# Kernel optimization log

Hardware: AMD Instinct MI355X
Metric: run time of the kernel (lower is better)

## Reference

```python
import jax, jax.numpy as jnp
import numpy as np

B, Q, K, D, H = 8, 128, 1024, 256, 256


def setup_inputs() -> dict:
    key = jax.random.key(0)
    ks = jax.random.split(key, 7)
    queries = jax.random.normal(ks[0], (B, Q, D), dtype=jnp.float32)
    keys = jax.random.normal(ks[1], (B, K, D), dtype=jnp.float32)
    values = jax.random.normal(ks[2], (B, K, D), dtype=jnp.float32)
    W_q = jax.random.normal(ks[3], (H, D), dtype=jnp.float32) * (1.0 / np.sqrt(D))
    W_k = jax.random.normal(ks[4], (H, D), dtype=jnp.float32) * (1.0 / np.sqrt(D))
    w_v = jax.random.normal(ks[5], (H,), dtype=jnp.float32) * (1.0 / np.sqrt(H))
    valid_lens = jax.random.randint(ks[6], (B,), 0, K, dtype=jnp.int64)
    return {"queries": queries, "keys": keys, "values": values,
            "W_q": W_q, "W_k": W_k, "w_v": w_v, "valid_lens": valid_lens}


def reference(queries, keys, values, W_q, W_k, w_v, valid_lens):
    # Linear projections (bias=False): [B,Q,H], [B,K,H]
    q = jnp.einsum("bqd,hd->bqh", queries, W_q)
    k = jnp.einsum("bkd,hd->bkh", keys, W_k)
    # Broadcast add -> tanh -> reduce with w_v: scores [B,Q,K]
    features = jnp.tanh(q[:, :, None, :] + k[:, None, :, :])  # [B,Q,K,H]
    scores = jnp.einsum("bqkh,h->bqk", features, w_v)
    # Masked softmax over K: positions >= valid_len get -1e9
    mask = jnp.arange(K)[None, None, :] < valid_lens[:, None, None]
    scores = jnp.where(mask, scores, jnp.float32(-1e9))
    attn = jax.nn.softmax(scores, axis=-1)  # [B,Q,K]
    # Dropout p=0.0 (eval): identity. bmm(attn, values) -> [B,Q,Dv]
    return jnp.einsum("bqk,bkv->bqv", attn, values)
```

## Files before the change

kernel.cpp:

```cpp
#include <hip/hip_runtime.h>

#define BB 8
#define QQ 128
#define KK 1024
#define DD 256
#define HH 256

#define KSP 32
#define KCH 32

#define ZSP 4
#define RTOT (BB * QQ + BB * KK)
#define PSTRIDE ((size_t)RTOT * HH)

#define TWO_LOG2E     2.8853900817779268f
#define NEG_TWO_LOG2E -2.8853900817779268f

__global__ __launch_bounds__(256) void proj_kernel(const float* __restrict__ queries,
                                                   const float* __restrict__ keys,
                                                   const float* __restrict__ Wq,
                                                   const float* __restrict__ Wk,
                                                   const int* __restrict__ vlen,
                                                   float* __restrict__ pp) {
    const int r0 = blockIdx.x * 64;
    const bool isQ = (r0 < BB * QQ);
    if (!isQ) {
        const int kb = (r0 - BB * QQ) >> 6;
        const int b  = kb >> 4;
        const int k0 = (kb & 15) << 6;
        if (k0 >= vlen[b]) return;
    }

    __shared__ float smem[192 * 68];
    float (*As)[68] = (float(*)[68])smem;
    float (*Ws)[68] = (float(*)[68])(smem + 64 * 68);

    const int t  = threadIdx.x;
    const int tr = t & 15;
    const int th = t >> 4;
    const int h0 = blockIdx.y * 128;
    const int dc = blockIdx.z * 64;
    const float* A = isQ ? (queries + (size_t)r0 * DD)
                         : (keys + (size_t)(r0 - BB * QQ) * DD);
    const float* W = isQ ? Wq : Wk;

#pragma unroll
    for (int i = 0; i < 4; ++i) {
        int fi  = t + 256 * i;
        int row = fi >> 4;
        int c4  = (fi & 15) << 2;
        *(float4*)&As[row][c4] = *(const float4*)&A[(size_t)row * DD + dc + c4];
    }
#pragma unroll
    for (int i = 0; i < 8; ++i) {
        int fi  = t + 256 * i;
        int row = fi >> 4;
        int c4  = (fi & 15) << 2;
        *(float4*)&Ws[row][c4] = *(const float4*)&W[(size_t)(h0 + row) * DD + dc + c4];
    }
    __syncthreads();

    float acc[4][8] = {};
#pragma unroll 2
    for (int dd = 0; dd < 64; dd += 4) {
        float4 a4[4], w4[8];
#pragma unroll
        for (int i = 0; i < 4; ++i) a4[i] = *(float4*)&As[tr + 16 * i][dd];
#pragma unroll
        for (int j = 0; j < 8; ++j) w4[j] = *(float4*)&Ws[th + 16 * j][dd];
#pragma unroll
        for (int i = 0; i < 4; ++i)
#pragma unroll
            for (int j = 0; j < 8; ++j) {
                acc[i][j] += a4[i].x * w4[j].x + a4[i].y * w4[j].y +
                             a4[i].z * w4[j].z + a4[i].w * w4[j].w;
            }
    }
    __syncthreads();

    float (*Ob)[132] = (float(*)[132])smem;
#pragma unroll
    for (int i = 0; i < 4; ++i)
#pragma unroll
        for (int j = 0; j < 8; ++j)
            Ob[tr + 16 * i][th + 16 * j] = TWO_LOG2E * acc[i][j];
    __syncthreads();

    float* outp = pp + (size_t)blockIdx.z * PSTRIDE + (size_t)r0 * HH + h0;
#pragma unroll
    for (int i = 0; i < 8; ++i) {
        int fi  = t + 256 * i;
        int row = fi >> 5;
        int c4  = (fi & 31) << 2;
        *(float4*)&outp[(size_t)row * HH + c4] = *(float4*)&Ob[row][c4];
    }
}

__global__ __launch_bounds__(256) void combine_kernel(const float* __restrict__ pp,
                                                      const int* __restrict__ vlen,
                                                      float* __restrict__ ppc) {
    const int row = blockIdx.x * 4 + (threadIdx.x >> 6);
    const int l   = threadIdx.x & 63;
    if (row >= BB * QQ) {
        const int rk = row - BB * QQ;
        const int b  = rk >> 10;
        const int k  = rk & (KK - 1);
        if (k >= vlen[b]) return;
    }
    const float* base = pp + (size_t)row * HH + (l << 2);
    float4 v0 = *(const float4*)base;
    float4 v1 = *(const float4*)(base + PSTRIDE);
    float4 v2 = *(const float4*)(base + 2 * PSTRIDE);
    float4 v3 = *(const float4*)(base + 3 * PSTRIDE);
    float4 s;
    s.x = __builtin_amdgcn_exp2f((v0.x + v1.x) + (v2.x + v3.x));
    s.y = __builtin_amdgcn_exp2f((v0.y + v1.y) + (v2.y + v3.y));
    s.z = __builtin_amdgcn_exp2f((v0.z + v1.z) + (v2.z + v3.z));
    s.w = __builtin_amdgcn_exp2f((v0.w + v1.w) + (v2.w + v3.w));
    *(float4*)&ppc[(size_t)row * HH + (l << 2)] = s;
}

__global__ __launch_bounds__(512, 4) void scoreav_kernel(const float* __restrict__ ppc,
                                                         const float* __restrict__ wv,
                                                         const int* __restrict__ vlen,
                                                         const float* __restrict__ V,
                                                         float* __restrict__ partial,
                                                         float* __restrict__ psum) {
    int id = blockIdx.x;
    int b = 0;
    bool found = false;
#pragma unroll
    for (int bb = 0; bb < BB; ++bb) {
        if (!found) {
            int v = vlen[bb];
            int cnt = ((v == 0) ? KSP : ((v + KCH - 1) / KCH)) * 4;
            if (id < cnt) { b = bb; found = true; }
            else id -= cnt;
        }
    }
    if (!found) return;
    const int ksb = id >> 2;
    const int q0  = (id & 3) * 32;
    const int k0  = ksb * KCH;
    const int vl  = vlen[b];

    __shared__ float st[2][32][260];
    __shared__ float pT[KCH][36];
    float* red = &st[0][0][0];

    const int t = threadIdx.x;
    const int w = t >> 6;
    const int l = t & 63;
    const int ql = l & 7;
    const int kl = l >> 3;

    float acc[4][4] = {};

    if (vl > 0) {
#pragma unroll
        for (int i = 0; i < 8; ++i) {
            int fi  = t + 512 * i;
            int row = fi >> 6;
            int c4  = (fi & 63) << 2;
            size_t gr = (row < 32) ? (size_t)(b * QQ + q0 + row)
                                   : (size_t)(BB * QQ + b * KK + k0 + row - 32);
            *(float4*)&st[row >> 5][row & 31][c4] =
                *(const float4*)&ppc[gr * HH + c4];
        }
        __syncthreads();

        const int hw = 32 * w;
#pragma unroll
        for (int hh = 0; hh < 32; hh += 4) {
            const float4 w4 = *(const float4*)&wv[hw + hh];
            const float* wa = (const float*)&w4;
            float4 q4[4], k4[4];
#pragma unroll
            for (int i = 0; i < 4; ++i) q4[i] = *(float4*)&st[0][ql + 8 * i][hw + hh];
#pragma unroll
            for (int j = 0; j < 4; ++j) k4[j] = *(float4*)&st[1][kl + 8 * j][hw + hh];
#pragma unroll
            for (int i = 0; i < 4; ++i) {
                const float* qa = (const float*)&q4[i];
#pragma unroll
                for (int j = 0; j < 4; ++j) {
                    const float* ka = (const float*)&k4[j];
#pragma unroll
                    for (int c = 0; c < 4; ++c) {
                        float d = __builtin_fmaf(qa[c], ka[c], 1.0f);
                        acc[i][j] += wa[c] * __builtin_amdgcn_rcpf(d);
                    }
                }
            }
        }
        __syncthreads();

#pragma unroll
        for (int i = 0; i < 4; ++i)
#pragma unroll
            for (int j = 0; j < 4; ++j)
                red[w * 1056 + (ql + 8 * i) * 33 + (kl + 8 * j)] = acc[i][j];
    }
    __syncthreads();

    float pvv[2];
#pragma unroll
    for (int u = 0; u < 2; ++u) {
        int n = t + 512 * u;
        int q = n >> 5, k = n & 31;
        float s = 0.f;
        if (vl > 0) {
#pragma unroll
            for (int ww = 0; ww < 8; ++ww) s += red[ww * 1056 + q * 33 + k];
        }
        int kg = k0 + k;
        float pv;
        if (vl == 0) pv = 1.0f;
        else pv = (kg < vl) ? __builtin_amdgcn_exp2f(NEG_TWO_LOG2E * s) : 0.0f;
        pT[k][q] = pv;
        pvv[u] = pv;
    }
    float s0 = pvv[0], s1 = pvv[1];
#pragma unroll
    for (int off = 1; off < 32; off <<= 1) {
        s0 += __shfl_xor(s0, off);
        s1 += __shfl_xor(s1, off);
    }
    if ((l & 31) == 0) {
        int qa = 2 * w + (l >> 5);
        psum[((size_t)ksb * BB + b) * QQ + q0 + qa]      = s0;
        psum[((size_t)ksb * BB + b) * QQ + q0 + qa + 16] = s1;
    }
    __syncthreads();

    const float* VB = V + ((size_t)b * KK + k0) * DD;
    const int d4 = (t & 63) << 2;
    const int qg = w << 2;
    float4 a4[4] = {};
#pragma unroll 4
    for (int k = 0; k < KCH; ++k) {
        float4 v4 = *(const float4*)&VB[(size_t)k * DD + d4];
        float4 p4 = *(float4*)&pT[k][qg];
        a4[0].x += p4.x * v4.x; a4[0].y += p4.x * v4.y; a4[0].z += p4.x * v4.z; a4[0].w += p4.x * v4.w;
        a4[1].x += p4.y * v4.x; a4[1].y += p4.y * v4.y; a4[1].z += p4.y * v4.z; a4[1].w += p4.y * v4.w;
        a4[2].x += p4.z * v4.x; a4[2].y += p4.z * v4.y; a4[2].z += p4.z * v4.z; a4[2].w += p4.z * v4.w;
        a4[3].x += p4.w * v4.x; a4[3].y += p4.w * v4.y; a4[3].z += p4.w * v4.z; a4[3].w += p4.w * v4.w;
    }
#pragma unroll
    for (int qi = 0; qi < 4; ++qi) {
        int q = q0 + qg + qi;
        *(float4*)&partial[(((size_t)ksb * BB + b) * QQ + q) * DD + d4] = a4[qi];
    }
}

__global__ __launch_bounds__(256) void av_reduce(const float* __restrict__ partial,
                                                 const float* __restrict__ psum,
                                                 const int* __restrict__ vlen,
                                                 float* __restrict__ out) {
    const int i  = blockIdx.x * 256 + threadIdx.x;
    const int bq = i >> 6;
    const int b  = bq >> 7;
    const int vl = vlen[b];
    const int nch = (vl == 0) ? KSP : ((vl + KCH - 1) / KCH);

    const float4* p4 = (const float4*)partial;
    const int stride4 = BB * QQ * DD / 4;

    float S = 0.f;
    float4 s = {0.f, 0.f, 0.f, 0.f};
    int ks = 0;
    for (; ks + 4 <= nch; ks += 4) {
        float Sa = psum[(size_t)(ks + 0) * (BB * QQ) + bq];
        float Sb = psum[(size_t)(ks + 1) * (BB * QQ) + bq];
        float Sc = psum[(size_t)(ks + 2) * (BB * QQ) + bq];
        float Sd = psum[(size_t)(ks + 3) * (BB * QQ) + bq];
        float4 x0 = p4[(size_t)(ks + 0) * stride4 + i];
        float4 x1 = p4[(size_t)(ks + 1) * stride4 + i];
        float4 x2 = p4[(size_t)(ks + 2) * stride4 + i];
        float4 x3 = p4[(size_t)(ks + 3) * stride4 + i];
        S += (Sa + Sb) + (Sc + Sd);
        s.x += (x0.x + x1.x) + (x2.x + x3.x);
        s.y += (x0.y + x1.y) + (x2.y + x3.y);
        s.z += (x0.z + x1.z) + (x2.z + x3.z);
        s.w += (x0.w + x1.w) + (x2.w + x3.w);
    }
    for (; ks < nch; ++ks) {
        S += psum[(size_t)ks * (BB * QQ) + bq];
        float4 x = p4[(size_t)ks * stride4 + i];
        s.x += x.x; s.y += x.y; s.z += x.z; s.w += x.w;
    }

    const float inv = 1.0f / S;
    s.x *= inv; s.y *= inv; s.z *= inv; s.w *= inv;
    ((float4*)out)[i] = s;
}

extern "C" void kernel_launch(void* const* d_in, const int* in_sizes, int n_in,
                              void* d_out, int out_size, void* d_ws, size_t ws_size,
                              hipStream_t stream) {
    const float* queries = (const float*)d_in[0];
    const float* keys    = (const float*)d_in[1];
    const float* values  = (const float*)d_in[2];
    const float* W_q     = (const float*)d_in[3];
    const float* W_k     = (const float*)d_in[4];
    const float* w_v     = (const float*)d_in[5];
    const int*   vlen    = (const int*)d_in[6];
    float* out = (float*)d_out;

    float* ws      = (float*)d_ws;
    float* pp      = ws;
    float* ppc     = pp + (size_t)ZSP * PSTRIDE;
    float* psum    = ppc + PSTRIDE;
    float* partial = psum + (size_t)KSP * BB * QQ;

    proj_kernel<<<dim3(RTOT / 64, HH / 128, ZSP), 256, 0, stream>>>(
        queries, keys, W_q, W_k, vlen, pp);

    combine_kernel<<<dim3(RTOT / 4, 1, 1), 256, 0, stream>>>(pp, vlen, ppc);

    scoreav_kernel<<<dim3(KSP * 4 * BB, 1, 1), 512, 0, stream>>>(
        ppc, w_v, vlen, values, partial, psum);

    av_reduce<<<dim3(BB * QQ * DD / 4 / 256, 1, 1), 256, 0, stream>>>(
        partial, psum, vlen, out);
}
```

Measured before the change: 129.8 us.

## Process two key chunks per score block and shrink projection tile

The score/AV kernel now loops over two 32-key chunks per block, accumulating the AV partials and softmax sums in registers, which halves the number of key splits and the partial/psum traffic the reduce kernel must read. The projection kernel's H tile drops from 128 to 64, doubling its grid and cutting per-thread accumulators to raise parallelism and occupancy. The cost is fewer, longer score blocks with extra barriers, and the projection's shared loads of the A tile are no longer shared across as many outputs.

```diff
diff --git a/kernel.cpp b/kernel.cpp
--- a/kernel.cpp
+++ b/kernel.cpp
@@ -6,7 +6,7 @@
 #define DD 256
 #define HH 256
 
-#define KSP 32
+#define NSC 16
 #define KCH 32
 
 #define ZSP 4
@@ -31,14 +31,14 @@
         if (k0 >= vlen[b]) return;
     }
 
-    __shared__ float smem[192 * 68];
+    __shared__ float smem[2 * 64 * 68];
     float (*As)[68] = (float(*)[68])smem;
     float (*Ws)[68] = (float(*)[68])(smem + 64 * 68);
 
     const int t  = threadIdx.x;
     const int tr = t & 15;
     const int th = t >> 4;
-    const int h0 = blockIdx.y * 128;
+    const int h0 = blockIdx.y * 64;
     const int dc = blockIdx.z * 64;
     const float* A = isQ ? (queries + (size_t)r0 * DD)
                          : (keys + (size_t)(r0 - BB * QQ) * DD);
@@ -50,48 +50,42 @@
         int row = fi >> 4;
         int c4  = (fi & 15) << 2;
         *(float4*)&As[row][c4] = *(const float4*)&A[(size_t)row * DD + dc + c4];
-    }
-#pragma unroll
-    for (int i = 0; i < 8; ++i) {
+        *(float4*)&Ws[row][c4] = *(const float4*)&W[(size_t)(h0 + row) * DD + dc + c4];
+    }
+    __syncthreads();
+
+    float acc[4][4] = {};
+#pragma unroll 2
+    for (int dd = 0; dd < 64; dd += 4) {
+        float4 a4[4], w4[4];
+#pragma unroll
+        for (int i = 0; i < 4; ++i) a4[i] = *(float4*)&As[tr + 16 * i][dd];
+#pragma unroll
+        for (int j = 0; j < 4; ++j) w4[j] = *(float4*)&Ws[th + 16 * j][dd];
+#pragma unroll
+        for (int i = 0; i < 4; ++i)
+#pragma unroll
+            for (int j = 0; j < 4; ++j) {
+                acc[i][j] += a4[i].x * w4[j].x + a4[i].y * w4[j].y +
+                             a4[i].z * w4[j].z + a4[i].w * w4[j].w;
+            }
+    }
+    __syncthreads();
+
+    float (*Ob)[68] = (float(*)[68])smem;
+#pragma unroll
+    for (int i = 0; i < 4; ++i)
+#pragma unroll
+        for (int j = 0; j < 4; ++j)
+            Ob[tr + 16 * i][th + 16 * j] = TWO_LOG2E * acc[i][j];
+    __syncthreads();
+
+    float* outp = pp + (size_t)blockIdx.z * PSTRIDE + (size_t)r0 * HH + h0;
+#pragma unroll
+    for (int i = 0; i < 4; ++i) {
         int fi  = t + 256 * i;
         int row = fi >> 4;
         int c4  = (fi & 15) << 2;
-        *(float4*)&Ws[row][c4] = *(const float4*)&W[(size_t)(h0 + row) * DD + dc + c4];
-    }
-    __syncthreads();
-
-    float acc[4][8] = {};
-#pragma unroll 2
-    for (int dd = 0; dd < 64; dd += 4) {
-        float4 a4[4], w4[8];
-#pragma unroll
-        for (int i = 0; i < 4; ++i) a4[i] = *(float4*)&As[tr + 16 * i][dd];
-#pragma unroll
-        for (int j = 0; j < 8; ++j) w4[j] = *(float4*)&Ws[th + 16 * j][dd];
-#pragma unroll
-        for (int i = 0; i < 4; ++i)
-#pragma unroll
-            for (int j = 0; j < 8; ++j) {
-                acc[i][j] += a4[i].x * w4[j].x + a4[i].y * w4[j].y +
-                             a4[i].z * w4[j].z + a4[i].w * w4[j].w;
-            }
-    }
-    __syncthreads();
-
-    float (*Ob)[132] = (float(*)[132])smem;
-#pragma unroll
-    for (int i = 0; i < 4; ++i)
-#pragma unroll
-        for (int j = 0; j < 8; ++j)
-            Ob[tr + 16 * i][th + 16 * j] = TWO_LOG2E * acc[i][j];
-    __syncthreads();
-
-    float* outp = pp + (size_t)blockIdx.z * PSTRIDE + (size_t)r0 * HH + h0;
-#pragma unroll
-    for (int i = 0; i < 8; ++i) {
-        int fi  = t + 256 * i;
-        int row = fi >> 5;
-        int c4  = (fi & 31) << 2;
         *(float4*)&outp[(size_t)row * HH + c4] = *(float4*)&Ob[row][c4];
     }
 }
@@ -133,7 +127,7 @@
     for (int bb = 0; bb < BB; ++bb) {
         if (!found) {
             int v = vlen[bb];
-            int cnt = ((v == 0) ? KSP : ((v + KCH - 1) / KCH)) * 4;
+            int cnt = ((v == 0) ? NSC : ((v + 63) >> 6)) * 4;
             if (id < cnt) { b = bb; found = true; }
             else id -= cnt;
         }
@@ -141,7 +135,7 @@
     if (!found) return;
     const int ksb = id >> 2;
     const int q0  = (id & 3) * 32;
-    const int k0  = ksb * KCH;
+    const int k0s = ksb * 64;
     const int vl  = vlen[b];
 
     __shared__ float st[2][32][260];
@@ -153,99 +147,119 @@
     const int l = t & 63;
     const int ql = l & 7;
     const int kl = l >> 3;
-
-    float acc[4][4] = {};
-
-    if (vl > 0) {
-#pragma unroll
-        for (int i = 0; i < 8; ++i) {
-            int fi  = t + 512 * i;
-            int row = fi >> 6;
-            int c4  = (fi & 63) << 2;
-            size_t gr = (row < 32) ? (size_t)(b * QQ + q0 + row)
-                                   : (size_t)(BB * QQ + b * KK + k0 + row - 32);
-            *(float4*)&st[row >> 5][row & 31][c4] =
-                *(const float4*)&ppc[gr * HH + c4];
-        }
-        __syncthreads();
-
-        const int hw = 32 * w;
-#pragma unroll
-        for (int hh = 0; hh < 32; hh += 4) {
-            const float4 w4 = *(const float4*)&wv[hw + hh];
-            const float* wa = (const float*)&w4;
-            float4 q4[4], k4[4];
-#pragma unroll
-            for (int i = 0; i < 4; ++i) q4[i] = *(float4*)&st[0][ql + 8 * i][hw + hh];
-#pragma unroll
-            for (int j = 0; j < 4; ++j) k4[j] = *(float4*)&st[1][kl + 8 * j][hw + hh];
-#pragma unroll
-            for (int i = 0; i < 4; ++i) {
-                const float* qa = (const float*)&q4[i];
-#pragma unroll
-                for (int j = 0; j < 4; ++j) {
-                    const float* ka = (const float*)&k4[j];
-#pragma unroll
-                    for (int c = 0; c < 4; ++c) {
-                        float d = __builtin_fmaf(qa[c], ka[c], 1.0f);
-                        acc[i][j] += wa[c] * __builtin_amdgcn_rcpf(d);
+    const int d4 = (t & 63) << 2;
+    const int qg = w << 2;
+
+    float4 a4[4] = {{0.f,0.f,0.f,0.f},{0.f,0.f,0.f,0.f},
+                    {0.f,0.f,0.f,0.f},{0.f,0.f,0.f,0.f}};
+    float sc0 = 0.f, sc1 = 0.f;
+
+#pragma unroll
+    for (int ck = 0; ck < 2; ++ck) {
+        const int k0 = k0s + 32 * ck;
+        const bool live = (vl > 0) && (k0 < vl);
+        float acc[4][4] = {};
+
+        if (live) {
+#pragma unroll
+            for (int i = 0; i < 8; ++i) {
+                int fi  = t + 512 * i;
+                int row = fi >> 6;
+                int c4  = (fi & 63) << 2;
+                size_t gr = (row < 32) ? (size_t)(b * QQ + q0 + row)
+                                       : (size_t)(BB * QQ + b * KK + k0 + row - 32);
+                *(float4*)&st[row >> 5][row & 31][c4] =
+                    *(const float4*)&ppc[gr * HH + c4];
+            }
+        }
+        __syncthreads();
+
+        if (live) {
+            const int hw = 32 * w;
+#pragma unroll
+            for (int hh = 0; hh < 32; hh += 4) {
+                const float4 w4 = *(const float4*)&wv[hw + hh];
+                const float* wa = (const float*)&w4;
+                float4 q4[4], k4[4];
+#pragma unroll
+                for (int i = 0; i < 4; ++i) q4[i] = *(float4*)&st[0][ql + 8 * i][hw + hh];
+#pragma unroll
+                for (int j = 0; j < 4; ++j) k4[j] = *(float4*)&st[1][kl + 8 * j][hw + hh];
+#pragma unroll
+                for (int i = 0; i < 4; ++i) {
+                    const float* qa = (const float*)&q4[i];
+#pragma unroll
+                    for (int j = 0; j < 4; ++j) {
+                        const float* ka = (const float*)&k4[j];
+#pragma unroll
+                        for (int c = 0; c < 4; ++c) {
+                            float d = __builtin_fmaf(qa[c], ka[c], 1.0f);
+                            acc[i][j] += wa[c] * __builtin_amdgcn_rcpf(d);
+                        }
                     }
                 }
             }
         }
         __syncthreads();
 
-#pragma unroll
-        for (int i = 0; i < 4; ++i)
-#pragma unroll
-            for (int j = 0; j < 4; ++j)
-                red[w * 1056 + (ql + 8 * i) * 33 + (kl + 8 * j)] = acc[i][j];
-    }
-    __syncthreads();
-
-    float pvv[2];
-#pragma unroll
-    for (int u = 0; u < 2; ++u) {
-        int n = t + 512 * u;
-        int q = n >> 5, k = n & 31;
-        float s = 0.f;
-        if (vl > 0) {
-#pragma unroll
-            for (int ww = 0; ww < 8; ++ww) s += red[ww * 1056 + q * 33 + k];
-        }
-        int kg = k0 + k;
-        float pv;
-        if (vl == 0) pv = 1.0f;
-        else pv = (kg < vl) ? __builtin_amdgcn_exp2f(NEG_TWO_LOG2E * s) : 0.0f;
-        pT[k][q] = pv;
-        pvv[u] = pv;
-    }
-    float s0 = pvv[0], s1 = pvv[1];
-#pragma unroll
-    for (int off = 1; off < 32; off <<= 1) {
-        s0 += __shfl_xor(s0, off);
-        s1 += __shfl_xor(s1, off);
-    }
+        if (live) {
+#pragma unroll
+            for (int i = 0; i < 4; ++i)
+#pragma unroll
+                for (int j = 0; j < 4; ++j)
+                    red[w * 1056 + (ql + 8 * i) * 33 + (kl + 8 * j)] = acc[i][j];
+        }
+        __syncthreads();
+
+        float pvv[2];
+#pragma unroll
+        for (int u = 0; u < 2; ++u) {
+            int n = t + 512 * u;
+            int q = n >> 5, k = n & 31;
+            float s = 0.f;
+            if (live) {
+#pragma unroll
+                for (int ww = 0; ww < 8; ++ww) s += red[ww * 1056 + q * 33 + k];
+            }
+            int kg = k0 + k;
+            float pv;
+            if (vl == 0) pv = 1.0f;
+            else pv = (live && kg < vl) ? __builtin_amdgcn_exp2f(NEG_TWO_LOG2E * s)
+                                        : 0.0f;
+            pT[k][q] = pv;
+            pvv[u] = pv;
+        }
+        float s0 = pvv[0], s1 = pvv[1];
+#pragma unroll
+        for (int off = 1; off < 32; off <<= 1) {
+            s0 += __shfl_xor(s0, off);
+            s1 += __shfl_xor(s1, off);
+        }
+        sc0 += s0;
+        sc1 += s1;
+        __syncthreads();
+
+        if (vl == 0 || live) {
+            const float* VB = V + ((size_t)b * KK + k0) * DD;
+#pragma unroll 4
+            for (int k = 0; k < KCH; ++k) {
+                float4 v4 = *(const float4*)&VB[(size_t)k * DD + d4];
+                float4 p4 = *(float4*)&pT[k][qg];
+                a4[0].x += p4.x * v4.x; a4[0].y += p4.x * v4.y; a4[0].z += p4.x * v4.z; a4[0].w += p4.x * v4.w;
+                a4[1].x += p4.y * v4.x; a4[1].y += p4.y * v4.y; a4[1].z += p4.y * v4.z; a4[1].w += p4.y * v4.w;
+                a4[2].x += p4.z * v4.x; a4[2].y += p4.z * v4.y; a4[2].z += p4.z * v4.z; a4[2].w += p4.z * v4.w;
+                a4[3].x += p4.w * v4.x; a4[3].y += p4.w * v4.y; a4[3].z += p4.w * v4.z; a4[3].w += p4.w * v4.w;
+            }
+        }
+        __syncthreads();
+    }
+
     if ((l & 31) == 0) {
         int qa = 2 * w + (l >> 5);
-        psum[((size_t)ksb * BB + b) * QQ + q0 + qa]      = s0;
-        psum[((size_t)ksb * BB + b) * QQ + q0 + qa + 16] = s1;
-    }
-    __syncthreads();
-
-    const float* VB = V + ((size_t)b * KK + k0) * DD;
-    const int d4 = (t & 63) << 2;
-    const int qg = w << 2;
-    float4 a4[4] = {};
-#pragma unroll 4
-    for (int k = 0; k < KCH; ++k) {
-        float4 v4 = *(const float4*)&VB[(size_t)k * DD + d4];
-        float4 p4 = *(float4*)&pT[k][qg];
-        a4[0].x += p4.x * v4.x; a4[0].y += p4.x * v4.y; a4[0].z += p4.x * v4.z; a4[0].w += p4.x * v4.w;
-        a4[1].x += p4.y * v4.x; a4[1].y += p4.y * v4.y; a4[1].z += p4.y * v4.z; a4[1].w += p4.y * v4.w;
-        a4[2].x += p4.z * v4.x; a4[2].y += p4.z * v4.y; a4[2].z += p4.z * v4.z; a4[2].w += p4.z * v4.w;
-        a4[3].x += p4.w * v4.x; a4[3].y += p4.w * v4.y; a4[3].z += p4.w * v4.z; a4[3].w += p4.w * v4.w;
-    }
+        psum[((size_t)ksb * BB + b) * QQ + q0 + qa]      = sc0;
+        psum[((size_t)ksb * BB + b) * QQ + q0 + qa + 16] = sc1;
+    }
+
 #pragma unroll
     for (int qi = 0; qi < 4; ++qi) {
         int q = q0 + qg + qi;
@@ -261,7 +275,7 @@
     const int bq = i >> 6;
     const int b  = bq >> 7;
     const int vl = vlen[b];
-    const int nch = (vl == 0) ? KSP : ((vl + KCH - 1) / KCH);
+    const int nch = (vl == 0) ? NSC : ((vl + 63) >> 6);
 
     const float4* p4 = (const float4*)partial;
     const int stride4 = BB * QQ * DD / 4;
@@ -311,14 +325,14 @@
     float* pp      = ws;
     float* ppc     = pp + (size_t)ZSP * PSTRIDE;
     float* psum    = ppc + PSTRIDE;
-    float* partial = psum + (size_t)KSP * BB * QQ;
-
-    proj_kernel<<<dim3(RTOT / 64, HH / 128, ZSP), 256, 0, stream>>>(
+    float* partial = psum + (size_t)NSC * BB * QQ;
+
+    proj_kernel<<<dim3(RTOT / 64, HH / 64, ZSP), 256, 0, stream>>>(
         queries, keys, W_q, W_k, vlen, pp);
 
     combine_kernel<<<dim3(RTOT / 4, 1, 1), 256, 0, stream>>>(pp, vlen, ppc);
 
-    scoreav_kernel<<<dim3(KSP * 4 * BB, 1, 1), 512, 0, stream>>>(
+    scoreav_kernel<<<dim3(NSC * 4 * BB, 1, 1), 512, 0, stream>>>(
         ppc, w_v, vlen, values, partial, psum);
 
     av_reduce<<<dim3(BB * QQ * DD / 4 / 256, 1, 1), 256, 0, stream>>>(
```

Result: slower. 227.8 us (+75.6%).
